# Performance work log

Measured on AMD Instinct MI355X. Metric: run time of the kernel, lower is better.

Reference implementation:

```python
import jax, jax.numpy as jnp
import numpy as np

B, T, U, D = 2, 256, 64, 512
INNER, VOCAB = 512, 4096


def setup_inputs() -> dict:
    key = jax.random.key(0)
    k1, k2, k3, k4, k5, k6 = jax.random.split(key, 6)
    s1 = 1.0 / np.sqrt(2 * D)      # torch Linear init scale for fan_in=2D
    s2 = 1.0 / np.sqrt(INNER)
    return {
        "enc_state": jax.random.normal(k1, (B, T, D), dtype=jnp.float32),
        "dec_state": jax.random.normal(k2, (B, U, D), dtype=jnp.float32),
        "W1": jax.random.normal(k3, (INNER, 2 * D), dtype=jnp.float32) * s1,
        "b1": jax.random.normal(k4, (INNER,), dtype=jnp.float32) * s1,
        "W2": jax.random.normal(k5, (VOCAB, INNER), dtype=jnp.float32) * s2,
        "b2": jax.random.normal(k6, (VOCAB,), dtype=jnp.float32) * s2,
    }


def reference(enc_state, dec_state, W1, b1, W2, b2):
    # JointNet: repeat enc (B,T,1,D)->(B,T,U,D), dec (B,1,U,D)->(B,T,U,D),
    # concat -> Linear(2D,inner) -> tanh -> Linear(inner,vocab).
    # Equivalent efficient form: split W1 into enc/dec halves, project each
    # sequence once, broadcast-add (the concat+Linear decomposes exactly).
    d = enc_state.shape[-1]
    We, Wd = W1[:, :d], W1[:, d:]
    enc_proj = jnp.einsum("btd,id->bti", enc_state, We)   # (B,T,inner)
    dec_proj = jnp.einsum("bud,id->bui", dec_state, Wd)   # (B,U,inner)
    h = jnp.tanh(enc_proj[:, :, None, :] + dec_proj[:, None, :, :] + b1)  # (B,T,U,inner)
    logits = jnp.einsum("btui,vi->btuv", h, W2) + b2       # (B,T,U,vocab)
    return logits
```

## Files before the change

### kernel.cpp

```cpp
#include <hip/hip_runtime.h>
#include <hip/hip_bf16.h>
#include <stdint.h>

#define T_DIM 256
#define U_DIM 64
#define D_DIM 512
#define NIN 512
#define NV 4096

typedef __bf16 bf16x8 __attribute__((ext_vector_type(8)));
typedef float f32x4 __attribute__((ext_vector_type(4)));

static __device__ __forceinline__ unsigned short f2bf(float x) {
  union { float f; unsigned int u; } v; v.f = x;
  unsigned int r = v.u + 0x7FFFu + ((v.u >> 16) & 1u);
  return (unsigned short)(r >> 16);
}

static __device__ __forceinline__ void gload_lds16(const unsigned short* g, void* l) {
  __builtin_amdgcn_global_load_lds(
      (__attribute__((address_space(1))) void*)(unsigned short*)g,
      (__attribute__((address_space(3))) void*)l, 16, 0, 0);
}

__global__ __launch_bounds__(256) void convert_w2_kernel(const float* __restrict__ W2,
                                                         unsigned short* __restrict__ W2b) {
  int q = blockIdx.x * 256 + threadIdx.x;
  const float4 v0 = *(const float4*)(W2 + (size_t)q * 8);
  const float4 v1 = *(const float4*)(W2 + (size_t)q * 8 + 4);
  union { unsigned short s[8]; uint4 u; } o;
  o.s[0] = f2bf(v0.x); o.s[1] = f2bf(v0.y); o.s[2] = f2bf(v0.z); o.s[3] = f2bf(v0.w);
  o.s[4] = f2bf(v1.x); o.s[5] = f2bf(v1.y); o.s[6] = f2bf(v1.z); o.s[7] = f2bf(v1.w);
  *(uint4*)(W2b + (size_t)q * 8) = o.u;
}

__global__ __launch_bounds__(256) void proj_kernel(const float* __restrict__ enc,
                                                   const float* __restrict__ dec,
                                                   const float* __restrict__ W1,
                                                   float* __restrict__ ep0,
                                                   float* __restrict__ ep1,
                                                   float* __restrict__ dp0,
                                                   float* __restrict__ dp1) {
  __shared__ unsigned short As[128 * 32];
  __shared__ unsigned short Bs[128 * 32];
  const int tid = threadIdx.x;
  const int tile_m = blockIdx.x >> 3;
  const int kh = (blockIdx.x >> 2) & 1;
  const int tile_n = blockIdx.x & 3;
  const bool is_dec = (tile_m == 4);
  const float* X = is_dec ? dec : enc;
  const int xrow0 = is_dec ? 0 : tile_m * 128;
  const int wcol0 = is_dec ? D_DIM : 0;
  float* outp = is_dec ? (kh ? dp1 : dp0) : (kh ? ep1 : ep0);

  const int lane = tid & 63;
  const int wv = tid >> 6;
  const int wr = wv >> 1, wc = wv & 1;

  const int arow = tid >> 1;
  const int acol = (tid & 1) * 16;

  f32x4 acc[4][4] = {};

  const float* pa = X + (size_t)(xrow0 + arow) * D_DIM + acol;
  const float* pb = W1 + (size_t)(tile_n * 128 + arow) * (2 * D_DIM) + wcol0 + acol;

  for (int k0 = kh * 256; k0 < kh * 256 + 256; k0 += 32) {
    float4 av0 = *(const float4*)(pa + k0);
    float4 av1 = *(const float4*)(pa + k0 + 4);
    float4 av2 = *(const float4*)(pa + k0 + 8);
    float4 av3 = *(const float4*)(pa + k0 + 12);
    float4 bv0 = *(const float4*)(pb + k0);
    float4 bv1 = *(const float4*)(pb + k0 + 4);
    float4 bv2 = *(const float4*)(pb + k0 + 8);
    float4 bv3 = *(const float4*)(pb + k0 + 12);
    __syncthreads();
    union { unsigned short s[8]; uint4 u; } u0, u1, w0, w1;
    u0.s[0] = f2bf(av0.x); u0.s[1] = f2bf(av0.y); u0.s[2] = f2bf(av0.z); u0.s[3] = f2bf(av0.w);
    u0.s[4] = f2bf(av1.x); u0.s[5] = f2bf(av1.y); u0.s[6] = f2bf(av1.z); u0.s[7] = f2bf(av1.w);
    u1.s[0] = f2bf(av2.x); u1.s[1] = f2bf(av2.y); u1.s[2] = f2bf(av2.z); u1.s[3] = f2bf(av2.w);
    u1.s[4] = f2bf(av3.x); u1.s[5] = f2bf(av3.y); u1.s[6] = f2bf(av3.z); u1.s[7] = f2bf(av3.w);
    w0.s[0] = f2bf(bv0.x); w0.s[1] = f2bf(bv0.y); w0.s[2] = f2bf(bv0.z); w0.s[3] = f2bf(bv0.w);
    w0.s[4] = f2bf(bv1.x); w0.s[5] = f2bf(bv1.y); w0.s[6] = f2bf(bv1.z); w0.s[7] = f2bf(bv1.w);
    w1.s[0] = f2bf(bv2.x); w1.s[1] = f2bf(bv2.y); w1.s[2] = f2bf(bv2.z); w1.s[3] = f2bf(bv2.w);
    w1.s[4] = f2bf(bv3.x); w1.s[5] = f2bf(bv3.y); w1.s[6] = f2bf(bv3.z); w1.s[7] = f2bf(bv3.w);
    *(uint4*)&As[arow * 32 + acol] = u0.u;
    *(uint4*)&As[arow * 32 + acol + 8] = u1.u;
    *(uint4*)&Bs[arow * 32 + acol] = w0.u;
    *(uint4*)&Bs[arow * 32 + acol + 8] = w1.u;
    __syncthreads();
    bf16x8 af[4], bff[4];
#pragma unroll
    for (int mi = 0; mi < 4; ++mi)
      af[mi] = *(const bf16x8*)&As[(wr * 64 + mi * 16 + (lane & 15)) * 32 + (lane >> 4) * 8];
#pragma unroll
    for (int ni = 0; ni < 4; ++ni)
      bff[ni] = *(const bf16x8*)&Bs[(wc * 64 + ni * 16 + (lane & 15)) * 32 + (lane >> 4) * 8];
#pragma unroll
    for (int mi = 0; mi < 4; ++mi)
#pragma unroll
      for (int ni = 0; ni < 4; ++ni)
        acc[mi][ni] = __builtin_amdgcn_mfma_f32_16x16x32_bf16(af[mi], bff[ni], acc[mi][ni], 0, 0, 0);
  }

#pragma unroll
  for (int mi = 0; mi < 4; ++mi) {
#pragma unroll
    for (int r = 0; r < 4; ++r) {
      int row = xrow0 + wr * 64 + mi * 16 + ((lane >> 4) << 2) + r;
      float* po = outp + (size_t)row * NIN + tile_n * 128 + wc * 64 + (lane & 15);
#pragma unroll
      for (int ni = 0; ni < 4; ++ni) po[ni * 16] = acc[mi][ni][r];
    }
  }
}

__global__ __launch_bounds__(256) void h_kernel(const float* __restrict__ ep0,
                                                const float* __restrict__ ep1,
                                                const float* __restrict__ dp0,
                                                const float* __restrict__ dp1,
                                                const float* __restrict__ b1,
                                                unsigned short* __restrict__ Hb) {
  int q = blockIdx.x * 256 + threadIdx.x;
  int m = q >> 6;
  int i0 = (q & 63) << 3;
  size_t eoff = (size_t)(m >> 6) * NIN + i0;
  size_t doff = (size_t)((m >> 14) * U_DIM + (m & 63)) * NIN + i0;
  float4 e0 = *(const float4*)(ep0 + eoff);
  float4 e1 = *(const float4*)(ep0 + eoff + 4);
  float4 f0 = *(const float4*)(ep1 + eoff);
  float4 f1 = *(const float4*)(ep1 + eoff + 4);
  float4 d0 = *(const float4*)(dp0 + doff);
  float4 d1 = *(const float4*)(dp0 + doff + 4);
  float4 g0 = *(const float4*)(dp1 + doff);
  float4 g1 = *(const float4*)(dp1 + doff + 4);
  float4 c0 = *(const float4*)(b1 + i0);
  float4 c1 = *(const float4*)(b1 + i0 + 4);
  float x[8] = { e0.x + f0.x + d0.x + g0.x + c0.x, e0.y + f0.y + d0.y + g0.y + c0.y,
                 e0.z + f0.z + d0.z + g0.z + c0.z, e0.w + f0.w + d0.w + g0.w + c0.w,
                 e1.x + f1.x + d1.x + g1.x + c1.x, e1.y + f1.y + d1.y + g1.y + c1.y,
                 e1.z + f1.z + d1.z + g1.z + c1.z, e1.w + f1.w + d1.w + g1.w + c1.w };
  union { unsigned short s[8]; uint4 u; } o;
#pragma unroll
  for (int j = 0; j < 8; ++j) {
    float ex = __expf(2.0f * x[j]);
    float t = 1.0f - 2.0f / (ex + 1.0f);
    o.s[j] = f2bf(t);
  }
  *(uint4*)(Hb + (size_t)q * 8) = o.u;
}

__global__ __launch_bounds__(512, 2) void gemm256_kernel(const unsigned short* __restrict__ Hb,
                                                         const unsigned short* __restrict__ W2b,
                                                         const float* __restrict__ b2,
                                                         float* __restrict__ out) {
  __shared__ __align__(16) char smem[131072];
  const int tid = threadIdx.x;
  const int bid = blockIdx.x;
  const int swz = ((bid & 7) << 8) | (bid >> 3);
  const int tile_n = swz & 15, tile_m = swz >> 4;
  const int m0 = tile_m * 256, n0 = tile_n * 256;
  const int lane = tid & 63, w = tid >> 6;
  const int wr = w >> 2, wc = w & 3;

  const int srow0 = (w << 4) + (lane >> 2);
  const int segp = ((((lane & 3) - ((lane >> 3) & 3)) & 3) << 3);
  const unsigned short* pA0 = Hb + (size_t)(m0 + srow0) * 512 + segp;
  const unsigned short* pA1 = pA0 + 128 * 512;
  const unsigned short* pB0 = W2b + (size_t)(n0 + srow0) * 512 + segp;
  const unsigned short* pB1 = pB0 + 128 * 512;
  const int dstOff = (w << 10) + (lane << 4);
  const int laneA = ((lane & 15) << 6) + ((((lane >> 4) + ((lane >> 1) & 7)) & 3) << 4);
  const int wrOff = wr << 13;
  const int wcOff = wc << 12;

  f32x4 acc[8][4] = {};
  bf16x8 af[8], bq0, bq1;

#define STAGE_A(BUF, KH, T) do { \
    gload_lds16(pA0 + (T) * 64 + (KH) * 32, smem + (BUF) * 32768 + (KH) * 16384 + dstOff); \
    gload_lds16(pA1 + (T) * 64 + (KH) * 32, smem + (BUF) * 32768 + (KH) * 16384 + 8192 + dstOff); \
  } while (0)
#define STAGE_B(BUF, KH, T) do { \
    gload_lds16(pB0 + (T) * 64 + (KH) * 32, smem + 65536 + (BUF) * 32768 + (KH) * 16384 + dstOff); \
    gload_lds16(pB1 + (T) * 64 + (KH) * 32, smem + 65536 + (BUF) * 32768 + (KH) * 16384 + 8192 + dstOff); \
  } while (0)
#define DS_A(BUF, KH, MI) (*(const bf16x8*)(smem + (BUF) * 32768 + (KH) * 16384 + wrOff + (MI) * 1024 + laneA))
#define DS_B(BUF, KH, NI) (*(const bf16x8*)(smem + 65536 + (BUF) * 32768 + (KH) * 16384 + wcOff + (NI) * 1024 + laneA))
#define LD_A(BUF, KH) do { \
    _Pragma("unroll") for (int mi = 0; mi < 8; ++mi) af[mi] = DS_A(BUF, KH, mi); \
  } while (0)
#define QUAD(NH) do { \
    __builtin_amdgcn_s_setprio(1); \
    _Pragma("unroll") for (int mi = 0; mi < 8; ++mi) { \
      acc[mi][2 * (NH)]     = __builtin_amdgcn_mfma_f32_16x16x32_bf16(af[mi], bq0, acc[mi][2 * (NH)], 0, 0, 0); \
      acc[mi][2 * (NH) + 1] = __builtin_amdgcn_mfma_f32_16x16x32_bf16(af[mi], bq1, acc[mi][2 * (NH) + 1], 0, 0, 0); \
    } \
    __builtin_amdgcn_s_setprio(0); \
  } while (0)
#define BAR() __builtin_amdgcn_s_barrier()
#define LGKM0() asm volatile("s_waitcnt lgkmcnt(0)" ::: "memory")
#define VMCNT4() asm volatile("s_waitcnt vmcnt(4)" ::: "memory")
#define VMCNT0() asm volatile("s_waitcnt vmcnt(0)" ::: "memory")

  STAGE_A(0, 0, 0); STAGE_A(0, 1, 0); STAGE_B(0, 0, 0); STAGE_B(0, 1, 0);
  STAGE_A(1, 0, 1); STAGE_B(1, 0, 1);
  VMCNT4();
  BAR();

  for (int i = 0; i < 3; ++i) {
    const int t1 = 2 * i + 1, t2 = 2 * i + 2, t3 = 2 * i + 3;
    LD_A(0, 0); bq0 = DS_B(0, 0, 0); bq1 = DS_B(0, 0, 1);
    STAGE_A(1, 1, t1);
    BAR(); LGKM0(); QUAD(0); BAR();
    bq0 = DS_B(0, 0, 2); bq1 = DS_B(0, 0, 3);
    STAGE_B(1, 1, t1);
    BAR(); LGKM0(); QUAD(1); BAR();
    LD_A(0, 1); bq0 = DS_B(0, 1, 0); bq1 = DS_B(0, 1, 1);
    STAGE_A(0, 0, t2);
    BAR(); LGKM0(); QUAD(0); BAR();
    bq0 = DS_B(0, 1, 2); bq1 = DS_B(0, 1, 3);
    STAGE_B(0, 0, t2);
    VMCNT4();
    BAR(); LGKM0(); QUAD(1); BAR();
    LD_A(1, 0); bq0 = DS_B(1, 0, 0); bq1 = DS_B(1, 0, 1);
    STAGE_A(0, 1, t2);
    BAR(); LGKM0(); QUAD(0); BAR();
    bq0 = DS_B(1, 0, 2); bq1 = DS_B(1, 0, 3);
    STAGE_B(0, 1, t2);
    BAR(); LGKM0(); QUAD(1); BAR();
    LD_A(1, 1); bq0 = DS_B(1, 1, 0); bq1 = DS_B(1, 1, 1);
    STAGE_A(1, 0, t3);
    BAR(); LGKM0(); QUAD(0); BAR();
    bq0 = DS_B(1, 1, 2); bq1 = DS_B(1, 1, 3);
    STAGE_B(1, 0, t3);
    VMCNT4();
    BAR(); LGKM0(); QUAD(1); BAR();
  }

  LD_A(0, 0); bq0 = DS_B(0, 0, 0); bq1 = DS_B(0, 0, 1);
  STAGE_A(1, 1, 7);
  BAR(); LGKM0(); QUAD(0); BAR();
  bq0 = DS_B(0, 0, 2); bq1 = DS_B(0, 0, 3);
  STAGE_B(1, 1, 7);
  BAR(); LGKM0(); QUAD(1); BAR();
  LD_A(0, 1); bq0 = DS_B(0, 1, 0); bq1 = DS_B(0, 1, 1);
  BAR(); LGKM0(); QUAD(0); BAR();
  bq0 = DS_B(0, 1, 2); bq1 = DS_B(0, 1, 3);
  VMCNT0();
  BAR(); LGKM0(); QUAD(1); BAR();
  LD_A(1, 0); bq0 = DS_B(1, 0, 0); bq1 = DS_B(1, 0, 1);
  BAR(); LGKM0(); QUAD(0); BAR();
  bq0 = DS_B(1, 0, 2); bq1 = DS_B(1, 0, 3);
  BAR(); LGKM0(); QUAD(1); BAR();
  LD_A(1, 1); bq0 = DS_B(1, 1, 0); bq1 = DS_B(1, 1, 1);
  BAR(); LGKM0(); QUAD(0); BAR();
  bq0 = DS_B(1, 1, 2); bq1 = DS_B(1, 1, 3);
  BAR(); LGKM0(); QUAD(1);

  float b2v[4];
#pragma unroll
  for (int ni = 0; ni < 4; ++ni) b2v[ni] = b2[n0 + wc * 64 + ni * 16 + (lane & 15)];
#pragma unroll
  for (int mi = 0; mi < 8; ++mi) {
#pragma unroll
    for (int r = 0; r < 4; ++r) {
      int row = m0 + wr * 128 + mi * 16 + ((lane >> 4) << 2) + r;
      float* po = out + (size_t)row * NV + n0 + wc * 64 + (lane & 15);
#pragma unroll
      for (int ni = 0; ni < 4; ++ni) po[ni * 16] = acc[mi][ni][r] + b2v[ni];
    }
  }
#undef STAGE_A
#undef STAGE_B
#undef DS_A
#undef DS_B
#undef LD_A
#undef QUAD
#undef BAR
#undef LGKM0
#undef VMCNT4
#undef VMCNT0
}

extern "C" void kernel_launch(void* const* d_in, const int* in_sizes, int n_in,
                              void* d_out, int out_size, void* d_ws, size_t ws_size,
                              hipStream_t stream) {
  const float* enc = (const float*)d_in[0];
  const float* dec = (const float*)d_in[1];
  const float* W1  = (const float*)d_in[2];
  const float* b1  = (const float*)d_in[3];
  const float* W2  = (const float*)d_in[4];
  const float* b2  = (const float*)d_in[5];
  float* out = (float*)d_out;

  char* ws = (char*)d_ws;
  unsigned short* W2b = (unsigned short*)(ws);
  float* ep0 = (float*)(ws + 4194304);
  float* ep1 = (float*)(ws + 5242880);
  float* dp0 = (float*)(ws + 6291456);
  float* dp1 = (float*)(ws + 6553600);
  unsigned short* Hb = (unsigned short*)(ws + 6815744);

  hipLaunchKernelGGL(convert_w2_kernel, dim3(1024), dim3(256), 0, stream, W2, W2b);
  hipLaunchKernelGGL(proj_kernel, dim3(40), dim3(256), 0, stream, enc, dec, W1, ep0, ep1, dp0, dp1);
  hipLaunchKernelGGL(h_kernel, dim3(8192), dim3(256), 0, stream, ep0, ep1, dp0, dp1, b1, Hb);
  hipLaunchKernelGGL(gemm256_kernel, dim3(2048), dim3(512), 0, stream, Hb, W2b, b2, out);
}
```

Measured before the change: 241.5 us.

## Replace tiled GEMM with persistent row-block kernel overlapping output stores with MFMA

The 2048-block 256x256-tile GEMM is replaced by 256 persistent blocks, each owning 128 rows of H and sweeping all 16 vocab column tiles. The previous tile's results, with bias added, are held in registers and stored in pieces interleaved with the next tile's MFMA work. The aim is to hide the large fp32 output write (about 537MB) behind compute and to reuse the A rows across tiles. The cost is a smaller 128x256 tile with lower arithmetic intensity, more registers for the held results, and only 256 blocks, which may not fill every CU evenly.

```diff
diff --git a/kernel.cpp b/kernel.cpp
--- a/kernel.cpp
+++ b/kernel.cpp
@@ -150,137 +150,151 @@
   *(uint4*)(Hb + (size_t)q * 8) = o.u;
 }
 
-__global__ __launch_bounds__(512, 2) void gemm256_kernel(const unsigned short* __restrict__ Hb,
-                                                         const unsigned short* __restrict__ W2b,
-                                                         const float* __restrict__ b2,
-                                                         float* __restrict__ out) {
-  __shared__ __align__(16) char smem[131072];
+__global__ __launch_bounds__(512, 2) void gemm_persist_kernel(const unsigned short* __restrict__ Hb,
+                                                              const unsigned short* __restrict__ W2b,
+                                                              const float* __restrict__ b2,
+                                                              float* __restrict__ outp) {
+  __shared__ __align__(16) char smem[98304];
   const int tid = threadIdx.x;
-  const int bid = blockIdx.x;
-  const int swz = ((bid & 7) << 8) | (bid >> 3);
-  const int tile_n = swz & 15, tile_m = swz >> 4;
-  const int m0 = tile_m * 256, n0 = tile_n * 256;
   const int lane = tid & 63, w = tid >> 6;
   const int wr = w >> 2, wc = w & 3;
+  const int m0 = blockIdx.x * 128;
 
   const int srow0 = (w << 4) + (lane >> 2);
   const int segp = ((((lane & 3) - ((lane >> 3) & 3)) & 3) << 3);
-  const unsigned short* pA0 = Hb + (size_t)(m0 + srow0) * 512 + segp;
-  const unsigned short* pA1 = pA0 + 128 * 512;
-  const unsigned short* pB0 = W2b + (size_t)(n0 + srow0) * 512 + segp;
-  const unsigned short* pB1 = pB0 + 128 * 512;
-  const int dstOff = (w << 10) + (lane << 4);
-  const int laneA = ((lane & 15) << 6) + ((((lane >> 4) + ((lane >> 1) & 7)) & 3) << 4);
-  const int wrOff = wr << 13;
-  const int wcOff = wc << 12;
-
-  f32x4 acc[8][4] = {};
-  bf16x8 af[8], bq0, bq1;
-
-#define STAGE_A(BUF, KH, T) do { \
-    gload_lds16(pA0 + (T) * 64 + (KH) * 32, smem + (BUF) * 32768 + (KH) * 16384 + dstOff); \
-    gload_lds16(pA1 + (T) * 64 + (KH) * 32, smem + (BUF) * 32768 + (KH) * 16384 + 8192 + dstOff); \
-  } while (0)
-#define STAGE_B(BUF, KH, T) do { \
-    gload_lds16(pB0 + (T) * 64 + (KH) * 32, smem + 65536 + (BUF) * 32768 + (KH) * 16384 + dstOff); \
-    gload_lds16(pB1 + (T) * 64 + (KH) * 32, smem + 65536 + (BUF) * 32768 + (KH) * 16384 + 8192 + dstOff); \
-  } while (0)
-#define DS_A(BUF, KH, MI) (*(const bf16x8*)(smem + (BUF) * 32768 + (KH) * 16384 + wrOff + (MI) * 1024 + laneA))
-#define DS_B(BUF, KH, NI) (*(const bf16x8*)(smem + 65536 + (BUF) * 32768 + (KH) * 16384 + wcOff + (NI) * 1024 + laneA))
-#define LD_A(BUF, KH) do { \
-    _Pragma("unroll") for (int mi = 0; mi < 8; ++mi) af[mi] = DS_A(BUF, KH, mi); \
-  } while (0)
-#define QUAD(NH) do { \
+  const unsigned short* pA = Hb + (size_t)(m0 + srow0) * 512 + segp;
+  const unsigned short* pB = W2b + (size_t)srow0 * 512 + segp;
+  const int dstOff = (w << 10) | (lane << 4);
+  const int laneA = ((lane & 15) << 6) | ((((lane >> 4) + ((lane >> 1) & 7)) & 3) << 4);
+
+  f32x4 acc[4][4] = {};
+  f32x4 old[4][4] = {};
+  float b2v[4];
+  bf16x8 af[4], bf[4];
+  size_t scol = 0;
+
+#define LDSA(b, k) (smem + (b) * 16384 + (k) * 8192)
+#define LDSB(b, k) (smem + 32768 + (b) * 32768 + (k) * 16384)
+#define BARR() __builtin_amdgcn_s_barrier()
+#define WAITVM_(N) asm volatile("s_waitcnt vmcnt(" #N ")" ::: "memory")
+#define WAITVM(N) WAITVM_(N)
+
+#define RD8(b, k) do { \
+    af[0] = *(const bf16x8*)(LDSA(b, k) + (wr << 12) + 0 + laneA); \
+    af[1] = *(const bf16x8*)(LDSA(b, k) + (wr << 12) + 1024 + laneA); \
+    af[2] = *(const bf16x8*)(LDSA(b, k) + (wr << 12) + 2048 + laneA); \
+    af[3] = *(const bf16x8*)(LDSA(b, k) + (wr << 12) + 3072 + laneA); \
+    bf[0] = *(const bf16x8*)(LDSB(b, k) + (wc << 12) + 0 + laneA); \
+    bf[1] = *(const bf16x8*)(LDSB(b, k) + (wc << 12) + 1024 + laneA); \
+    bf[2] = *(const bf16x8*)(LDSB(b, k) + (wc << 12) + 2048 + laneA); \
+    bf[3] = *(const bf16x8*)(LDSB(b, k) + (wc << 12) + 3072 + laneA); \
+  } while (0)
+
+#define QUAD16() do { \
     __builtin_amdgcn_s_setprio(1); \
-    _Pragma("unroll") for (int mi = 0; mi < 8; ++mi) { \
-      acc[mi][2 * (NH)]     = __builtin_amdgcn_mfma_f32_16x16x32_bf16(af[mi], bq0, acc[mi][2 * (NH)], 0, 0, 0); \
-      acc[mi][2 * (NH) + 1] = __builtin_amdgcn_mfma_f32_16x16x32_bf16(af[mi], bq1, acc[mi][2 * (NH) + 1], 0, 0, 0); \
-    } \
+    _Pragma("unroll") for (int mi = 0; mi < 4; ++mi) \
+      _Pragma("unroll") for (int ni = 0; ni < 4; ++ni) \
+        acc[mi][ni] = __builtin_amdgcn_mfma_f32_16x16x32_bf16(af[mi], bf[ni], acc[mi][ni], 0, 0, 0); \
     __builtin_amdgcn_s_setprio(0); \
   } while (0)
-#define BAR() __builtin_amdgcn_s_barrier()
-#define LGKM0() asm volatile("s_waitcnt lgkmcnt(0)" ::: "memory")
-#define VMCNT4() asm volatile("s_waitcnt vmcnt(4)" ::: "memory")
-#define VMCNT0() asm volatile("s_waitcnt vmcnt(0)" ::: "memory")
-
-  STAGE_A(0, 0, 0); STAGE_A(0, 1, 0); STAGE_B(0, 0, 0); STAGE_B(0, 1, 0);
-  STAGE_A(1, 0, 1); STAGE_B(1, 0, 1);
-  VMCNT4();
-  BAR();
-
-  for (int i = 0; i < 3; ++i) {
-    const int t1 = 2 * i + 1, t2 = 2 * i + 2, t3 = 2 * i + 3;
-    LD_A(0, 0); bq0 = DS_B(0, 0, 0); bq1 = DS_B(0, 0, 1);
-    STAGE_A(1, 1, t1);
-    BAR(); LGKM0(); QUAD(0); BAR();
-    bq0 = DS_B(0, 0, 2); bq1 = DS_B(0, 0, 3);
-    STAGE_B(1, 1, t1);
-    BAR(); LGKM0(); QUAD(1); BAR();
-    LD_A(0, 1); bq0 = DS_B(0, 1, 0); bq1 = DS_B(0, 1, 1);
-    STAGE_A(0, 0, t2);
-    BAR(); LGKM0(); QUAD(0); BAR();
-    bq0 = DS_B(0, 1, 2); bq1 = DS_B(0, 1, 3);
-    STAGE_B(0, 0, t2);
-    VMCNT4();
-    BAR(); LGKM0(); QUAD(1); BAR();
-    LD_A(1, 0); bq0 = DS_B(1, 0, 0); bq1 = DS_B(1, 0, 1);
-    STAGE_A(0, 1, t2);
-    BAR(); LGKM0(); QUAD(0); BAR();
-    bq0 = DS_B(1, 0, 2); bq1 = DS_B(1, 0, 3);
-    STAGE_B(0, 1, t2);
-    BAR(); LGKM0(); QUAD(1); BAR();
-    LD_A(1, 1); bq0 = DS_B(1, 1, 0); bq1 = DS_B(1, 1, 1);
-    STAGE_A(1, 0, t3);
-    BAR(); LGKM0(); QUAD(0); BAR();
-    bq0 = DS_B(1, 1, 2); bq1 = DS_B(1, 1, 3);
-    STAGE_B(1, 0, t3);
-    VMCNT4();
-    BAR(); LGKM0(); QUAD(1); BAR();
-  }
-
-  LD_A(0, 0); bq0 = DS_B(0, 0, 0); bq1 = DS_B(0, 0, 1);
-  STAGE_A(1, 1, 7);
-  BAR(); LGKM0(); QUAD(0); BAR();
-  bq0 = DS_B(0, 0, 2); bq1 = DS_B(0, 0, 3);
-  STAGE_B(1, 1, 7);
-  BAR(); LGKM0(); QUAD(1); BAR();
-  LD_A(0, 1); bq0 = DS_B(0, 1, 0); bq1 = DS_B(0, 1, 1);
-  BAR(); LGKM0(); QUAD(0); BAR();
-  bq0 = DS_B(0, 1, 2); bq1 = DS_B(0, 1, 3);
-  VMCNT0();
-  BAR(); LGKM0(); QUAD(1); BAR();
-  LD_A(1, 0); bq0 = DS_B(1, 0, 0); bq1 = DS_B(1, 0, 1);
-  BAR(); LGKM0(); QUAD(0); BAR();
-  bq0 = DS_B(1, 0, 2); bq1 = DS_B(1, 0, 3);
-  BAR(); LGKM0(); QUAD(1); BAR();
-  LD_A(1, 1); bq0 = DS_B(1, 1, 0); bq1 = DS_B(1, 1, 1);
-  BAR(); LGKM0(); QUAD(0); BAR();
-  bq0 = DS_B(1, 1, 2); bq1 = DS_B(1, 1, 3);
-  BAR(); LGKM0(); QUAD(1);
-
-  float b2v[4];
-#pragma unroll
-  for (int ni = 0; ni < 4; ++ni) b2v[ni] = b2[n0 + wc * 64 + ni * 16 + (lane & 15)];
-#pragma unroll
-  for (int mi = 0; mi < 8; ++mi) {
-#pragma unroll
-    for (int r = 0; r < 4; ++r) {
-      int row = m0 + wr * 128 + mi * 16 + ((lane >> 4) << 2) + r;
-      float* po = out + (size_t)row * NV + n0 + wc * 64 + (lane & 15);
-#pragma unroll
-      for (int ni = 0; ni < 4; ++ni) po[ni * 16] = acc[mi][ni][r] + b2v[ni];
+
+#define STORE2(T, PH) do { \
+    constexpr int F_ = 2 * (T) + (PH); \
+    constexpr int MI_ = F_ >> 2, NI_ = F_ & 3; \
+    float* po = outp + (size_t)(m0 + wr * 64 + MI_ * 16 + ((lane >> 4) << 2)) * NV \
+                + scol + (wc << 6) + (NI_ << 4) + (lane & 15); \
+    _Pragma("unroll") for (int r = 0; r < 4; ++r) po[(size_t)r * NV] = old[MI_][NI_][r]; \
+  } while (0)
+
+#define TILE(T, S, W2N, W1N) do { \
+    const int cb1 = (((T) + 1) & 7) << 6; \
+    const int nboff1 = (nt + (((T) == 7) ? 1 : 0)) << 17; \
+     \
+    gload_lds16(pA + cb1,      LDSA(((T) + 1) & 1, 0) + dstOff); \
+    gload_lds16(pA + cb1 + 32, LDSA(((T) + 1) & 1, 1) + dstOff); \
+    gload_lds16(pB + nboff1 + cb1,         LDSB(((T) + 1) & 1, 0) + dstOff); \
+    gload_lds16(pB + nboff1 + cb1 + 65536, LDSB(((T) + 1) & 1, 0) + 8192 + dstOff); \
+    RD8((T) & 1, 0); \
+    QUAD16(); \
+    if (S) { STORE2(T, 0); } \
+    WAITVM(W2N); BARR(); \
+     \
+    gload_lds16(pB + nboff1 + cb1 + 32,         LDSB(((T) + 1) & 1, 1) + dstOff); \
+    gload_lds16(pB + nboff1 + cb1 + 32 + 65536, LDSB(((T) + 1) & 1, 1) + 8192 + dstOff); \
+    RD8((T) & 1, 1); \
+    QUAD16(); \
+    if (S) { STORE2(T, 1); } \
+    WAITVM(W1N); BARR(); \
+  } while (0)
+
+#define B2LOAD(NT) do { \
+    _Pragma("unroll") for (int ni = 0; ni < 4; ++ni) \
+      b2v[ni] = b2[((NT) << 8) + (wc << 6) + (ni << 4) + (lane & 15)]; \
+  } while (0)
+
+#define BOUND() do { \
+    _Pragma("unroll") for (int mi = 0; mi < 4; ++mi) \
+      _Pragma("unroll") for (int ni = 0; ni < 4; ++ni) { \
+        _Pragma("unroll") for (int r = 0; r < 4; ++r) old[mi][ni][r] = acc[mi][ni][r] + b2v[ni]; \
+        acc[mi][ni] = (f32x4){0.f, 0.f, 0.f, 0.f}; \
+      } \
+  } while (0)
+
+  gload_lds16(pA + 0,  LDSA(0, 0) + dstOff);
+  gload_lds16(pA + 32, LDSA(0, 1) + dstOff);
+  gload_lds16(pB + 0,          LDSB(0, 0) + dstOff);
+  gload_lds16(pB + 65536,      LDSB(0, 0) + 8192 + dstOff);
+  gload_lds16(pB + 32,         LDSB(0, 1) + dstOff);
+  gload_lds16(pB + 32 + 65536, LDSB(0, 1) + 8192 + dstOff);
+  WAITVM(0); BARR();
+
+  {
+    const int nt = 0;
+    B2LOAD(0);
+    TILE(0, 0, 4, 2); TILE(1, 0, 4, 2); TILE(2, 0, 4, 2); TILE(3, 0, 4, 2);
+    TILE(4, 0, 4, 2); TILE(5, 0, 4, 2); TILE(6, 0, 4, 2); TILE(7, 0, 4, 2);
+    BOUND();
+  }
+  {
+    const int nt = 1;
+    B2LOAD(1);
+    scol = 0;
+    TILE(0, 1, 8, 10);
+    TILE(1, 1, 12, 10); TILE(2, 1, 12, 10); TILE(3, 1, 12, 10);
+    TILE(4, 1, 12, 10); TILE(5, 1, 12, 10); TILE(6, 1, 12, 10); TILE(7, 1, 12, 10);
+    BOUND();
+  }
+  for (int nt = 2; nt < 16; ++nt) {
+    B2LOAD(nt);
+    scol = (size_t)(nt - 1) << 8;
+    TILE(0, 1, 12, 10); TILE(1, 1, 12, 10); TILE(2, 1, 12, 10); TILE(3, 1, 12, 10);
+    TILE(4, 1, 12, 10); TILE(5, 1, 12, 10); TILE(6, 1, 12, 10); TILE(7, 1, 12, 10);
+    BOUND();
+  }
+
+  scol = (size_t)15 << 8;
+#pragma unroll
+  for (int mi = 0; mi < 4; ++mi) {
+#pragma unroll
+    for (int ni = 0; ni < 4; ++ni) {
+      float* po = outp + (size_t)(m0 + wr * 64 + mi * 16 + ((lane >> 4) << 2)) * NV
+                  + scol + (wc << 6) + (ni << 4) + (lane & 15);
+#pragma unroll
+      for (int r = 0; r < 4; ++r) po[(size_t)r * NV] = old[mi][ni][r];
     }
   }
-#undef STAGE_A
-#undef STAGE_B
-#undef DS_A
-#undef DS_B
-#undef LD_A
-#undef QUAD
-#undef BAR
-#undef LGKM0
-#undef VMCNT4
-#undef VMCNT0
+
+#undef LDSA
+#undef LDSB
+#undef BARR
+#undef WAITVM_
+#undef WAITVM
+#undef RD8
+#undef QUAD16
+#undef STORE2
+#undef TILE
+#undef B2LOAD
+#undef BOUND
 }
 
 extern "C" void kernel_launch(void* const* d_in, const int* in_sizes, int n_in,
@@ -305,5 +319,5 @@
   hipLaunchKernelGGL(convert_w2_kernel, dim3(1024), dim3(256), 0, stream, W2, W2b);
   hipLaunchKernelGGL(proj_kernel, dim3(40), dim3(256), 0, stream, enc, dec, W1, ep0, ep1, dp0, dp1);
   hipLaunchKernelGGL(h_kernel, dim3(8192), dim3(256), 0, stream, ep0, ep1, dp0, dp1, b1, Hb);
-  hipLaunchKernelGGL(gemm256_kernel, dim3(2048), dim3(512), 0, stream, Hb, W2b, b2, out);
-}
+  hipLaunchKernelGGL(gemm_persist_kernel, dim3(256), dim3(512), 0, stream, Hb, W2b, b2, out);
+}
```

Measured after the change: 281.8 us. +16.7%, slower.
